# Optimization experiments

Measured on AMD Instinct MI355X. Metric: run time of the kernel, lower is better.

Reference implementation:

```python
import jax, jax.numpy as jnp
import numpy as np

TEMPERATURE = 8.0
BIAS_WEIGHT = 1.0
NEG_FILL = -10000.0


def setup_inputs() -> dict:
    key = jax.random.key(0)
    k1, k2, k3, k4, k5 = jax.random.split(key, 5)
    B, H, S, D = 2, 12, 2048, 64
    q = jax.random.normal(k1, (B, H, S, D), dtype=jnp.float32)
    k = jax.random.normal(k2, (B, H, S, D), dtype=jnp.float32)
    v = jax.random.normal(k3, (B, H, S, D), dtype=jnp.float32)
    mask = jax.random.randint(k4, (B, 1, 1, S), 0, 2, dtype=jnp.int32)
    bias = jax.random.normal(k5, (1, H, S, S), dtype=jnp.float32)
    return {"q": q, "k": k, "v": v, "mask": mask, "bias": bias}


def reference(q, k, v, mask, bias):
    # attn = (q / T) @ k^T + bias * w   -> [B,H,S,S]
    attn = jnp.einsum("bhqd,bhkd->bhqk", q / TEMPERATURE, k)
    attn = attn + bias * BIAS_WEIGHT
    attn = jnp.where(mask == 0, NEG_FILL, attn)
    attn = jax.nn.softmax(attn, axis=-1)  # dropout p=0 (eval) -> identity
    out = jnp.einsum("bhqk,bhkd->bhqd", attn, v)
    return (out, attn)
```

## Files before the change

kernel.cpp:

```cpp
#include <hip/hip_runtime.h>

#define S_ 2048
#define D_ 64
#define H_ 12
#define TQB 16
#define CK 128
#define NCH (S_/CK)

typedef __attribute__((ext_vector_type(8))) short bf16x8;
typedef __attribute__((ext_vector_type(4))) float f32x4;

__device__ __forceinline__ unsigned short f2bf(float x) {
    unsigned u = __float_as_uint(x);
    return (unsigned short)((u + 0x7FFFu + ((u >> 16) & 1u)) >> 16);
}

#define STAGE(dst, srcp) {                                                  \
    const int key_ = tid >> 1, hf_ = tid & 1;                               \
    const float4* gp_ = (const float4*)((srcp) + (size_t)key_ * D_) + hf_*8;\
    float4 f_[8];                                                           \
    _Pragma("unroll") for (int i_ = 0; i_ < 8; ++i_) f_[i_] = gp_[i_];      \
    _Pragma("unroll") for (int g_ = 0; g_ < 4; ++g_) {                      \
        bf16x8 o_;                                                          \
        _Pragma("unroll") for (int e_ = 0; e_ < 8; ++e_)                    \
            o_[e_] = (short)f2bf(((const float*)f_)[g_*8 + e_]);            \
        int idx_ = (key_*64 + hf_*32 + g_*8) ^ ((key_ & 7) << 3);           \
        *(bf16x8*)&dst[idx_] = o_;                                          \
    } }

__global__ __launch_bounds__(256, 4) void sdpa_bias_kernel(
    const float* __restrict__ qm, const float* __restrict__ km,
    const float* __restrict__ vm, const int* __restrict__ mask,
    const float* __restrict__ bias, float* __restrict__ out,
    float* __restrict__ attn)
{
    const int tid  = threadIdx.x;
    const int lane = tid & 63;
    const int w    = tid >> 6;
    const int col  = lane & 15;
    const int lg   = lane >> 4;

    const int bhp = blockIdx.y;
    const int h = bhp >> 1, b = bhp & 1;
    const int bh = b * H_ + h;
    const int q0 = blockIdx.x * TQB;

    __shared__ __align__(16) short qs_s[TQB * D_];
    __shared__ __align__(16) short ks_s[CK * D_];
    __shared__ __align__(16) short vs_s[CK * D_];
    __shared__ __align__(16) short ps_s[4 * TQB * 40];
    __shared__ float sums_s[4][TQB];
    __shared__ float invs_s[TQB];

    if (tid < 64) {
        int row = tid >> 2, c4 = tid & 3;
        const float4* qp = (const float4*)(qm + ((size_t)bh * S_ + q0 + row) * D_) + c4*4;
        float4 f[4];
        #pragma unroll
        for (int i = 0; i < 4; ++i) f[i] = qp[i];
        #pragma unroll
        for (int g = 0; g < 2; ++g) {
            bf16x8 o;
            #pragma unroll
            for (int e = 0; e < 8; ++e)
                o[e] = (short)f2bf(((const float*)f)[g*8 + e] * 0.125f);
            int idx = (row*64 + c4*16 + g*8) ^ ((row & 7) << 3);
            *(bf16x8*)&qs_s[idx] = o;
        }
    }
    __syncthreads();

    bf16x8 qa0 = *(const bf16x8*)&qs_s[(col*64 +  0 + lg*8) ^ ((col & 7) << 3)];
    bf16x8 qa1 = *(const bf16x8*)&qs_s[(col*64 + 32 + lg*8) ^ ((col & 7) << 3)];

    const int*   mp = mask + (size_t)b * S_;
    const float* bb = bias + (size_t)h * S_ * S_;
    const float* kbase = km + (size_t)bh * S_ * D_;
    const float* vbase = vm + (size_t)bh * S_ * D_;

    float srow[4] = {0.f, 0.f, 0.f, 0.f};
    for (int ch = 0; ch < NCH; ++ch) {
        __syncthreads();
        STAGE(ks_s, kbase + (size_t)ch * CK * D_);
        __syncthreads();
        #pragma unroll
        for (int sub = 0; sub < 2; ++sub) {
            int kl = w*32 + sub*16 + col;
            int gk = ch*CK + kl;
            bf16x8 b0 = *(const bf16x8*)&ks_s[(kl*64 +  0 + lg*8) ^ ((kl & 7) << 3)];
            bf16x8 b1 = *(const bf16x8*)&ks_s[(kl*64 + 32 + lg*8) ^ ((kl & 7) << 3)];
            f32x4 c = {0.f, 0.f, 0.f, 0.f};
            c = __builtin_amdgcn_mfma_f32_16x16x32_bf16(qa0, b0, c, 0, 0, 0);
            c = __builtin_amdgcn_mfma_f32_16x16x32_bf16(qa1, b1, c, 0, 0, 0);
            int m = mp[gk];
            #pragma unroll
            for (int i = 0; i < 4; ++i) {
                int row = lg*4 + i;
                float lv = c[i] + __builtin_nontemporal_load(bb + (size_t)(q0+row)*S_ + gk);
                float e = m ? __expf(lv) : 0.f;
                srow[i] += e;
            }
        }
    }
    #pragma unroll
    for (int i = 0; i < 4; ++i) {
        float t = srow[i];
        t += __shfl_xor(t, 1, 64); t += __shfl_xor(t, 2, 64);
        t += __shfl_xor(t, 4, 64); t += __shfl_xor(t, 8, 64);
        srow[i] = t;
    }
    if (col == 0) {
        #pragma unroll
        for (int i = 0; i < 4; ++i) sums_s[w][lg*4 + i] = srow[i];
    }
    __syncthreads();
    if (tid < TQB)
        invs_s[tid] = 1.f / (sums_s[0][tid] + sums_s[1][tid]
                           + sums_s[2][tid] + sums_s[3][tid]);
    __syncthreads();
    float inv[4];
    #pragma unroll
    for (int i = 0; i < 4; ++i) inv[i] = invs_s[lg*4 + i];

    f32x4 oacc[4];
    #pragma unroll
    for (int d = 0; d < 4; ++d) oacc[d] = (f32x4){0.f, 0.f, 0.f, 0.f};
    short* psw = &ps_s[w * TQB * 40];
    float* arow = attn + ((size_t)bh * S_ + q0) * S_;

    for (int ch = 0; ch < NCH; ++ch) {
        __syncthreads();
        STAGE(ks_s, kbase + (size_t)ch * CK * D_);
        STAGE(vs_s, vbase + (size_t)ch * CK * D_);
        __syncthreads();
        #pragma unroll
        for (int sub = 0; sub < 2; ++sub) {
            int kl = w*32 + sub*16 + col;
            int gk = ch*CK + kl;
            bf16x8 b0 = *(const bf16x8*)&ks_s[(kl*64 +  0 + lg*8) ^ ((kl & 7) << 3)];
            bf16x8 b1 = *(const bf16x8*)&ks_s[(kl*64 + 32 + lg*8) ^ ((kl & 7) << 3)];
            f32x4 c = {0.f, 0.f, 0.f, 0.f};
            c = __builtin_amdgcn_mfma_f32_16x16x32_bf16(qa0, b0, c, 0, 0, 0);
            c = __builtin_amdgcn_mfma_f32_16x16x32_bf16(qa1, b1, c, 0, 0, 0);
            int m = mp[gk];
            #pragma unroll
            for (int i = 0; i < 4; ++i) {
                int row = lg*4 + i;
                float lv = c[i] + __builtin_nontemporal_load(bb + (size_t)(q0+row)*S_ + gk);
                float e = m ? __expf(lv) : 0.f;
                psw[row*40 + sub*16 + col] = (short)f2bf(e);
                __builtin_nontemporal_store(e * inv[i], arow + (size_t)row * S_ + gk);
            }
        }
        bf16x8 pa = *(const bf16x8*)&psw[col*40 + lg*8];
        #pragma unroll
        for (int dt = 0; dt < 4; ++dt) {
            bf16x8 vb;
            #pragma unroll
            for (int e = 0; e < 8; ++e) {
                int key = w*32 + lg*8 + e;
                vb[e] = vs_s[(key*64 + dt*16 + col) ^ ((key & 7) << 3)];
            }
            oacc[dt] = __builtin_amdgcn_mfma_f32_16x16x32_bf16(pa, vb, oacc[dt], 0, 0, 0);
        }
    }

    __syncthreads();
    float* ob = (float*)ks_s;
    #pragma unroll
    for (int dt = 0; dt < 4; ++dt)
        #pragma unroll
        for (int i = 0; i < 4; ++i)
            ob[w*1024 + (lg*4 + i)*64 + dt*16 + col] = oacc[dt][i];
    __syncthreads();
    float* op = out + ((size_t)bh * S_ + q0) * D_;
    for (int id = tid; id < TQB * D_; id += 256) {
        int q = id >> 6, d = id & 63;
        op[(size_t)q * D_ + d] = (ob[q*64 + d] + ob[1024 + q*64 + d]
                                + ob[2048 + q*64 + d] + ob[3072 + q*64 + d]) * invs_s[q];
    }
}

extern "C" void kernel_launch(void* const* d_in, const int* in_sizes, int n_in,
                              void* d_out, int out_size, void* d_ws, size_t ws_size,
                              hipStream_t stream) {
    const float* q    = (const float*)d_in[0];
    const float* k    = (const float*)d_in[1];
    const float* v    = (const float*)d_in[2];
    const int*   mask = (const int*)d_in[3];
    const float* bias = (const float*)d_in[4];
    float* out  = (float*)d_out;
    float* attn = out + (size_t)2 * H_ * S_ * D_;

    dim3 grid(S_ / TQB, 2 * H_);
    sdpa_bias_kernel<<<grid, 256, 0, stream>>>(q, k, v, mask, bias, out, attn);
}
```

Baseline: 1.426 ms.

## Replace two-pass softmax with single pass plus separate normalization kernel

Removes the first pass over K and bias that computed the row sums, so the bias and K chunks are now read once instead of twice. The unnormalized exp values go to attn, and the per-row inverse sums are written to workspace. A second elementwise kernel then rescales the whole attn tensor. This trades one full re-read of bias, plus its recompute, for an extra read and write of the 400MB attn output.

```diff
diff --git a/kernel.cpp b/kernel.cpp
--- a/kernel.cpp
+++ b/kernel.cpp
@@ -32,7 +32,7 @@
     const float* __restrict__ qm, const float* __restrict__ km,
     const float* __restrict__ vm, const int* __restrict__ mask,
     const float* __restrict__ bias, float* __restrict__ out,
-    float* __restrict__ attn)
+    float* __restrict__ attn, float* __restrict__ ws)
 {
     const int tid  = threadIdx.x;
     const int lane = tid & 63;
@@ -78,53 +78,10 @@
     const float* kbase = km + (size_t)bh * S_ * D_;
     const float* vbase = vm + (size_t)bh * S_ * D_;
 
-    float srow[4] = {0.f, 0.f, 0.f, 0.f};
-    for (int ch = 0; ch < NCH; ++ch) {
-        __syncthreads();
-        STAGE(ks_s, kbase + (size_t)ch * CK * D_);
-        __syncthreads();
-        #pragma unroll
-        for (int sub = 0; sub < 2; ++sub) {
-            int kl = w*32 + sub*16 + col;
-            int gk = ch*CK + kl;
-            bf16x8 b0 = *(const bf16x8*)&ks_s[(kl*64 +  0 + lg*8) ^ ((kl & 7) << 3)];
-            bf16x8 b1 = *(const bf16x8*)&ks_s[(kl*64 + 32 + lg*8) ^ ((kl & 7) << 3)];
-            f32x4 c = {0.f, 0.f, 0.f, 0.f};
-            c = __builtin_amdgcn_mfma_f32_16x16x32_bf16(qa0, b0, c, 0, 0, 0);
-            c = __builtin_amdgcn_mfma_f32_16x16x32_bf16(qa1, b1, c, 0, 0, 0);
-            int m = mp[gk];
-            #pragma unroll
-            for (int i = 0; i < 4; ++i) {
-                int row = lg*4 + i;
-                float lv = c[i] + __builtin_nontemporal_load(bb + (size_t)(q0+row)*S_ + gk);
-                float e = m ? __expf(lv) : 0.f;
-                srow[i] += e;
-            }
-        }
-    }
-    #pragma unroll
-    for (int i = 0; i < 4; ++i) {
-        float t = srow[i];
-        t += __shfl_xor(t, 1, 64); t += __shfl_xor(t, 2, 64);
-        t += __shfl_xor(t, 4, 64); t += __shfl_xor(t, 8, 64);
-        srow[i] = t;
-    }
-    if (col == 0) {
-        #pragma unroll
-        for (int i = 0; i < 4; ++i) sums_s[w][lg*4 + i] = srow[i];
-    }
-    __syncthreads();
-    if (tid < TQB)
-        invs_s[tid] = 1.f / (sums_s[0][tid] + sums_s[1][tid]
-                           + sums_s[2][tid] + sums_s[3][tid]);
-    __syncthreads();
-    float inv[4];
-    #pragma unroll
-    for (int i = 0; i < 4; ++i) inv[i] = invs_s[lg*4 + i];
-
     f32x4 oacc[4];
     #pragma unroll
     for (int d = 0; d < 4; ++d) oacc[d] = (f32x4){0.f, 0.f, 0.f, 0.f};
+    float srow[4] = {0.f, 0.f, 0.f, 0.f};
     short* psw = &ps_s[w * TQB * 40];
     float* arow = attn + ((size_t)bh * S_ + q0) * S_;
 
@@ -149,7 +106,8 @@
                 float lv = c[i] + __builtin_nontemporal_load(bb + (size_t)(q0+row)*S_ + gk);
                 float e = m ? __expf(lv) : 0.f;
                 psw[row*40 + sub*16 + col] = (short)f2bf(e);
-                __builtin_nontemporal_store(e * inv[i], arow + (size_t)row * S_ + gk);
+                __builtin_nontemporal_store(e, arow + (size_t)row * S_ + gk);
+                srow[i] += e;
             }
         }
         bf16x8 pa = *(const bf16x8*)&psw[col*40 + lg*8];
@@ -165,7 +123,26 @@
         }
     }
 
+    #pragma unroll
+    for (int i = 0; i < 4; ++i) {
+        float t = srow[i];
+        t += __shfl_xor(t, 1, 64); t += __shfl_xor(t, 2, 64);
+        t += __shfl_xor(t, 4, 64); t += __shfl_xor(t, 8, 64);
+        srow[i] = t;
+    }
+    if (col == 0) {
+        #pragma unroll
+        for (int i = 0; i < 4; ++i) sums_s[w][lg*4 + i] = srow[i];
+    }
     __syncthreads();
+    if (tid < TQB) {
+        float iv = 1.f / (sums_s[0][tid] + sums_s[1][tid]
+                        + sums_s[2][tid] + sums_s[3][tid]);
+        invs_s[tid] = iv;
+        ws[(size_t)bh * S_ + q0 + tid] = iv;
+    }
+    __syncthreads();
+
     float* ob = (float*)ks_s;
     #pragma unroll
     for (int dt = 0; dt < 4; ++dt)
@@ -181,6 +158,21 @@
     }
 }
 
+__global__ __launch_bounds__(256, 8) void attn_norm_kernel(
+    float* __restrict__ attn, const float* __restrict__ ws)
+{
+    const size_t total4 = (size_t)2 * H_ * S_ * S_ / 4;
+    const size_t stride = (size_t)gridDim.x * 256;
+    f32x4* a4 = (f32x4*)attn;
+    for (size_t i = (size_t)blockIdx.x * 256 + threadIdx.x; i < total4; i += stride) {
+        int r = (int)((i * 4) >> 11);
+        float iv = ws[r];
+        f32x4 t = __builtin_nontemporal_load(&a4[i]);
+        t *= iv;
+        __builtin_nontemporal_store(t, &a4[i]);
+    }
+}
+
 extern "C" void kernel_launch(void* const* d_in, const int* in_sizes, int n_in,
                               void* d_out, int out_size, void* d_ws, size_t ws_size,
                               hipStream_t stream) {
@@ -191,7 +183,9 @@
     const float* bias = (const float*)d_in[4];
     float* out  = (float*)d_out;
     float* attn = out + (size_t)2 * H_ * S_ * D_;
+    float* ws   = (float*)d_ws;
 
     dim3 grid(S_ / TQB, 2 * H_);
-    sdpa_bias_kernel<<<grid, 256, 0, stream>>>(q, k, v, mask, bias, out, attn);
+    sdpa_bias_kernel<<<grid, 256, 0, stream>>>(q, k, v, mask, bias, out, attn, ws);
+    attn_norm_kernel<<<dim3(2048), 256, 0, stream>>>(attn, ws);
 }
```

Measured after the change: 1.219 ms. 14.5% less time.

## Fuse softmax passes into one by caching bf16 exponentials in registers

Applied to the files above, without the earlier changes.

Merges the two passes over keys into one: the first pass now stages V as well, accumulates the PV product with unnormalized probabilities, and keeps every exponential packed as bf16 in a 64-register array. The attention matrix is then written from those registers scaled by the inverse row sum, so the second QK^T, the second bias read and the second K load are gone. The cost is heavy register pressure (occupancy bound lowered from 4 to 3) and attention values stored with only bf16 precision, which may exceed tolerance.

```diff
diff --git a/kernel.cpp b/kernel.cpp
--- a/kernel.cpp
+++ b/kernel.cpp
@@ -28,7 +28,7 @@
         *(bf16x8*)&dst[idx_] = o_;                                          \
     } }
 
-__global__ __launch_bounds__(256, 4) void sdpa_bias_kernel(
+__global__ __launch_bounds__(256, 3) void sdpa_bias_kernel(
     const float* __restrict__ qm, const float* __restrict__ km,
     const float* __restrict__ vm, const int* __restrict__ mask,
     const float* __restrict__ bias, float* __restrict__ out,
@@ -78,10 +78,18 @@
     const float* kbase = km + (size_t)bh * S_ * D_;
     const float* vbase = vm + (size_t)bh * S_ * D_;
 
+    f32x4 oacc[4];
+    #pragma unroll
+    for (int d = 0; d < 4; ++d) oacc[d] = (f32x4){0.f, 0.f, 0.f, 0.f};
     float srow[4] = {0.f, 0.f, 0.f, 0.f};
+    unsigned epk[NCH][2][2];
+    short* psw = &ps_s[w * TQB * 40];
+
+    #pragma unroll
     for (int ch = 0; ch < NCH; ++ch) {
         __syncthreads();
         STAGE(ks_s, kbase + (size_t)ch * CK * D_);
+        STAGE(vs_s, vbase + (size_t)ch * CK * D_);
         __syncthreads();
         #pragma unroll
         for (int sub = 0; sub < 2; ++sub) {
@@ -93,15 +101,32 @@
             c = __builtin_amdgcn_mfma_f32_16x16x32_bf16(qa0, b0, c, 0, 0, 0);
             c = __builtin_amdgcn_mfma_f32_16x16x32_bf16(qa1, b1, c, 0, 0, 0);
             int m = mp[gk];
+            unsigned short us[4];
             #pragma unroll
             for (int i = 0; i < 4; ++i) {
                 int row = lg*4 + i;
                 float lv = c[i] + __builtin_nontemporal_load(bb + (size_t)(q0+row)*S_ + gk);
                 float e = m ? __expf(lv) : 0.f;
+                us[i] = f2bf(e);
+                psw[row*40 + sub*16 + col] = (short)us[i];
                 srow[i] += e;
             }
+            epk[ch][sub][0] = (unsigned)us[0] | ((unsigned)us[1] << 16);
+            epk[ch][sub][1] = (unsigned)us[2] | ((unsigned)us[3] << 16);
+        }
+        bf16x8 pa = *(const bf16x8*)&psw[col*40 + lg*8];
+        #pragma unroll
+        for (int dt = 0; dt < 4; ++dt) {
+            bf16x8 vb;
+            #pragma unroll
+            for (int e = 0; e < 8; ++e) {
+                int key = w*32 + lg*8 + e;
+                vb[e] = vs_s[(key*64 + dt*16 + col) ^ ((key & 7) << 3)];
+            }
+            oacc[dt] = __builtin_amdgcn_mfma_f32_16x16x32_bf16(pa, vb, oacc[dt], 0, 0, 0);
         }
     }
+
     #pragma unroll
     for (int i = 0; i < 4; ++i) {
         float t = srow[i];
@@ -122,50 +147,24 @@
     #pragma unroll
     for (int i = 0; i < 4; ++i) inv[i] = invs_s[lg*4 + i];
 
-    f32x4 oacc[4];
+    float* arow = attn + ((size_t)bh * S_ + q0) * S_;
     #pragma unroll
-    for (int d = 0; d < 4; ++d) oacc[d] = (f32x4){0.f, 0.f, 0.f, 0.f};
-    short* psw = &ps_s[w * TQB * 40];
-    float* arow = attn + ((size_t)bh * S_ + q0) * S_;
-
     for (int ch = 0; ch < NCH; ++ch) {
-        __syncthreads();
-        STAGE(ks_s, kbase + (size_t)ch * CK * D_);
-        STAGE(vs_s, vbase + (size_t)ch * CK * D_);
-        __syncthreads();
         #pragma unroll
         for (int sub = 0; sub < 2; ++sub) {
-            int kl = w*32 + sub*16 + col;
-            int gk = ch*CK + kl;
-            bf16x8 b0 = *(const bf16x8*)&ks_s[(kl*64 +  0 + lg*8) ^ ((kl & 7) << 3)];
-            bf16x8 b1 = *(const bf16x8*)&ks_s[(kl*64 + 32 + lg*8) ^ ((kl & 7) << 3)];
-            f32x4 c = {0.f, 0.f, 0.f, 0.f};
-            c = __builtin_amdgcn_mfma_f32_16x16x32_bf16(qa0, b0, c, 0, 0, 0);
-            c = __builtin_amdgcn_mfma_f32_16x16x32_bf16(qa1, b1, c, 0, 0, 0);
-            int m = mp[gk];
-            #pragma unroll
-            for (int i = 0; i < 4; ++i) {
-                int row = lg*4 + i;
-                float lv = c[i] + __builtin_nontemporal_load(bb + (size_t)(q0+row)*S_ + gk);
-                float e = m ? __expf(lv) : 0.f;
-                psw[row*40 + sub*16 + col] = (short)f2bf(e);
-                __builtin_nontemporal_store(e * inv[i], arow + (size_t)row * S_ + gk);
-            }
-        }
-        bf16x8 pa = *(const bf16x8*)&psw[col*40 + lg*8];
-        #pragma unroll
-        for (int dt = 0; dt < 4; ++dt) {
-            bf16x8 vb;
-            #pragma unroll
-            for (int e = 0; e < 8; ++e) {
-                int key = w*32 + lg*8 + e;
-                vb[e] = vs_s[(key*64 + dt*16 + col) ^ ((key & 7) << 3)];
-            }
-            oacc[dt] = __builtin_amdgcn_mfma_f32_16x16x32_bf16(pa, vb, oacc[dt], 0, 0, 0);
+            int gk = ch*CK + w*32 + sub*16 + col;
+            unsigned u0 = epk[ch][sub][0], u1 = epk[ch][sub][1];
+            __builtin_nontemporal_store(__uint_as_float(u0 << 16)         * inv[0],
+                                        arow + (size_t)(lg*4 + 0) * S_ + gk);
+            __builtin_nontemporal_store(__uint_as_float(u0 & 0xFFFF0000u) * inv[1],
+                                        arow + (size_t)(lg*4 + 1) * S_ + gk);
+            __builtin_nontemporal_store(__uint_as_float(u1 << 16)         * inv[2],
+                                        arow + (size_t)(lg*4 + 2) * S_ + gk);
+            __builtin_nontemporal_store(__uint_as_float(u1 & 0xFFFF0000u) * inv[3],
+                                        arow + (size_t)(lg*4 + 3) * S_ + gk);
         }
     }
 
-    __syncthreads();
     float* ob = (float*)ks_s;
     #pragma unroll
     for (int dt = 0; dt < 4; ++dt)
```

Measured after the change: 1.391 ms. -2.4%, faster.
